# Kernel tuning notes

Hardware: AMD Instinct MI355X
Metric: run time of the kernel (lower is better)

Reference implementation:

```python
import jax, jax.numpy as jnp
import numpy as np

B, T, C, H = 256, 256, 384, 64
MAX_REL = 3  # max_relative_position hardcoded in module


def setup_inputs() -> dict:
    key = jax.random.key(0)
    ks = jax.random.split(key, 6)
    s = 1.0 / np.sqrt(C)
    return {
        "x": jax.random.normal(ks[0], (B, T, C), dtype=jnp.float32),
        "Wq": jax.random.normal(ks[1], (C, H), dtype=jnp.float32) * s,
        "Wk": jax.random.normal(ks[2], (C, H), dtype=jnp.float32) * s,
        "Wv": jax.random.normal(ks[3], (C, H), dtype=jnp.float32) * s,
        "rel_k_table": jax.random.normal(ks[4], (2 * MAX_REL + 1, H), dtype=jnp.float32) * s,
        "rel_v_table": jax.random.normal(ks[5], (2 * MAX_REL + 1, H), dtype=jnp.float32) * s,
    }


def reference(x, Wq, Wk, Wv, rel_k_table, rel_v_table):
    Bd, Td, Cd = x.shape
    Hd = Wq.shape[1]
    q = x @ Wq  # [B,T,H]
    k = x @ Wk
    v = x @ Wv
    # relative position indices, clipped Shaw-style
    r = jnp.arange(Td)
    idx = jnp.clip(r[None, :] - r[:, None], -MAX_REL, MAX_REL) + MAX_REL  # [T,T]
    rk = rel_k_table[idx]  # [T,T,H]
    rv = rel_v_table[idx]  # [T,T,H]
    attn1 = jnp.einsum('bth,bsh->bts', q, k)
    attn2 = jnp.einsum('bth,tsh->bts', q, rk)
    scale = jnp.sqrt(jnp.asarray(Hd, dtype=x.dtype))
    scores = (attn1 + attn2) / scale
    causal = jnp.tril(jnp.ones((Td, Td), dtype=bool))
    scores = jnp.where(causal[None, :, :], scores, -jnp.inf)
    attn = jax.nn.softmax(scores, axis=-1)  # dropout = identity (eval mode)
    w1 = jnp.einsum('bts,bsh->bth', attn, v)
    w2 = jnp.einsum('bts,tsh->bth', attn, rv)
    return w1 + w2  # [B,T,H]
```

## Files before the change

### kernel.cpp

```cpp
#include <hip/hip_runtime.h>
#include <hip/hip_bf16.h>


typedef __attribute__((ext_vector_type(8))) __bf16 bf16x8;
typedef __attribute__((ext_vector_type(8))) short short8;
typedef __attribute__((ext_vector_type(4))) float f32x4;
typedef __attribute__((ext_vector_type(4))) int   i32x4;

#define MFMA16(A, B, C) __builtin_amdgcn_mfma_f32_16x16x32_bf16((A), (B), (C), 0, 0, 0)

__device__ __forceinline__ unsigned short f2bf(float f) {
    unsigned int u = __builtin_bit_cast(unsigned int, f);
    u = (u + 0x7FFFu + ((u >> 16) & 1u)) >> 16;
    return (unsigned short)u;
}
__device__ __forceinline__ float bf2f(unsigned short s) {
    unsigned int u = ((unsigned int)s) << 16;
    return __builtin_bit_cast(float, u);
}
__device__ __forceinline__ bf16x8 ld16(const unsigned short* p) {
    return __builtin_bit_cast(bf16x8, *(const i32x4*)p);
}

__global__ void prep_wt(const float* __restrict__ Wq, const float* __restrict__ Wk,
                        const float* __restrict__ Wv, const float* __restrict__ relk,
                        unsigned short* __restrict__ Wt, unsigned short* __restrict__ Rk) {
    int i = blockIdx.x * 256 + threadIdx.x;
    if (i < 3 * 64 * 384) {
        int kk = i % 384;
        int h  = (i / 384) & 63;
        int w  = i / (384 * 64);
        const float* W = (w == 0) ? Wq : ((w == 1) ? Wk : Wv);
        Wt[i] = f2bf(W[kk * 64 + h]);
    } else if (i < 3 * 64 * 384 + 1024) {
        int j = i - 3 * 64 * 384;
        int n = j >> 6, h = j & 63;
        Rk[j] = (n < 4) ? f2bf(relk[n * 64 + h]) : (unsigned short)0;
    }
}

__global__ __launch_bounds__(512) void qkv_kernel(
        const float* __restrict__ x, const unsigned short* __restrict__ Wt,
        unsigned short* __restrict__ q, unsigned short* __restrict__ k,
        unsigned short* __restrict__ vT) {
    __shared__ unsigned short wlds[192][136];

    const int tid  = threadIdx.x;
    const int wave = tid >> 6;
    const int lane = tid & 63;
    const int c    = lane & 15;
    const int quad = lane >> 4;
    const int M0   = blockIdx.x * 128;
    const int myrow = M0 + wave * 16 + c;

    f32x4 zero = {0.f, 0.f, 0.f, 0.f};
    f32x4 aq[4], ak[4], av[4];
#pragma unroll
    for (int i = 0; i < 4; i++) { aq[i] = zero; ak[i] = zero; av[i] = zero; }

    for (int ck = 0; ck < 3; ck++) {
        if (ck) __syncthreads();
#pragma unroll
        for (int it = 0; it < 6; it++) {
            int i = it * 512 + tid;
            int r = i >> 4, kc = i & 15;
            i32x4 d = *(const i32x4*)(Wt + r * 384 + ck * 128 + kc * 8);
            *(i32x4*)(&wlds[r][kc * 8]) = d;
        }
        __syncthreads();

#pragma unroll
        for (int ks = 0; ks < 4; ks++) {
            const float* xp = x + (size_t)myrow * 384 + ck * 128 + ks * 32 + quad * 8;
            f32x4 x0 = *(const f32x4*)xp;
            f32x4 x1 = *(const f32x4*)(xp + 4);
            short8 xs;
#pragma unroll
            for (int j = 0; j < 4; j++) {
                xs[j]     = (short)f2bf(x0[j]);
                xs[4 + j] = (short)f2bf(x1[j]);
            }
            bf16x8 a = __builtin_bit_cast(bf16x8, xs);

#pragma unroll
            for (int nt = 0; nt < 8; nt++) {
                bf16x8 b = ld16(&wlds[nt * 16 + c][ks * 32 + quad * 8]);
                if (nt < 4) aq[nt]     = MFMA16(a, b, aq[nt]);
                else        ak[nt - 4] = MFMA16(a, b, ak[nt - 4]);
            }
#pragma unroll
            for (int mt = 0; mt < 4; mt++) {
                bf16x8 aw = ld16(&wlds[128 + mt * 16 + c][ks * 32 + quad * 8]);
                av[mt] = MFMA16(aw, a, av[mt]);
            }
        }
    }

    const int b   = M0 >> 8;
    const int t0b = M0 & 255;
#pragma unroll
    for (int nt = 0; nt < 4; nt++) {
#pragma unroll
        for (int r = 0; r < 4; r++) {
            int row = M0 + wave * 16 + quad * 4 + r;
            q[row * 64 + nt * 16 + c] = f2bf(aq[nt][r]);
            k[row * 64 + nt * 16 + c] = f2bf(ak[nt][r]);
        }
    }
#pragma unroll
    for (int mt = 0; mt < 4; mt++) {
#pragma unroll
        for (int r = 0; r < 4; r++) {
            int h = mt * 16 + quad * 4 + r;
            vT[(b * 64 + h) * 256 + t0b + wave * 16 + c] = f2bf(av[mt][r]);
        }
    }
}

__global__ __launch_bounds__(64, 4) void attn_kernel(
        const unsigned short* __restrict__ q, const unsigned short* __restrict__ k,
        const unsigned short* __restrict__ vT, const unsigned short* __restrict__ Rk,
        const float* __restrict__ relv, float* __restrict__ out) {
    __shared__ unsigned short P[16][264];
    __shared__ float E[16][4];

    const int lane = threadIdx.x;
    const int c    = lane & 15;
    const int quad = lane >> 4;
    const int tt   = blockIdx.x;
    const int b    = blockIdx.y;
    const int t0   = tt * 16;
    const int nst  = tt + 1;

    f32x4 zero = {0.f, 0.f, 0.f, 0.f};

    float rv[4][4];
#pragma unroll
    for (int j = 0; j < 4; j++)
#pragma unroll
        for (int nt = 0; nt < 4; nt++) rv[j][nt] = relv[j * 64 + nt * 16 + c];

    const unsigned short* qp = q + (size_t)(b * 256 + t0 + c) * 64 + quad * 8;
    bf16x8 aq0 = ld16(qp);
    bf16x8 aq1 = ld16(qp + 32);

    {
        f32x4 e = zero;
        e = MFMA16(aq0, ld16(Rk + c * 64 + quad * 8), e);
        e = MFMA16(aq1, ld16(Rk + c * 64 + 32 + quad * 8), e);
        if (c < 4) {
#pragma unroll
            for (int r = 0; r < 4; r++) E[quad * 4 + r][c] = e[r];
        }
    }
    __syncthreads();
    f32x4 ef[4];
#pragma unroll
    for (int r = 0; r < 4; r++) ef[r] = *(const f32x4*)(&E[quad * 4 + r][0]);

    float l[4] = {0.f, 0.f, 0.f, 0.f};
#pragma unroll
    for (int st = 0; st < 16; st++) {
        if (st < nst) {
            const unsigned short* kp = k + (size_t)(b * 256 + st * 16 + c) * 64 + quad * 8;
            f32x4 s = zero;
            s = MFMA16(aq0, ld16(kp), s);
            s = MFMA16(aq1, ld16(kp + 32), s);
#pragma unroll
            for (int r = 0; r < 4; r++) {
                int tg = t0 + quad * 4 + r;
                int sg = st * 16 + c;
                int d  = sg - tg;
                float e = (d <= -3) ? ef[r][0] : (d == -2) ? ef[r][1]
                        : (d == -1) ? ef[r][2] : ef[r][3];
                float p = (d > 0) ? 0.f : __expf(0.125f * (s[r] + e));
                l[r] += p;
                P[quad * 4 + r][sg] = f2bf(p);
            }
        }
    }
    if (nst & 1) {
#pragma unroll
        for (int r = 0; r < 4; r++) P[quad * 4 + r][nst * 16 + c] = 0;
    }
#pragma unroll
    for (int r = 0; r < 4; r++)
#pragma unroll
        for (int ofs = 1; ofs < 16; ofs <<= 1)
            l[r] += __shfl_xor(l[r], ofs, 64);
    float rl[4];
#pragma unroll
    for (int r = 0; r < 4; r++) rl[r] = 1.0f / l[r];
    __syncthreads();

    f32x4 o[4];
#pragma unroll
    for (int nt = 0; nt < 4; nt++) o[nt] = zero;
    const int ksteps = (nst + 1) >> 1;
#pragma unroll
    for (int ks = 0; ks < 8; ks++) {
        if (ks < ksteps) {
            bf16x8 ap = ld16(&P[c][ks * 32 + quad * 8]);
#pragma unroll
            for (int nt = 0; nt < 4; nt++) {
                const unsigned short* vp = vT + (size_t)(b * 64 + nt * 16 + c) * 256
                                              + ks * 32 + quad * 8;
                o[nt] = MFMA16(ap, ld16(vp), o[nt]);
            }
        }
    }

#pragma unroll
    for (int r = 0; r < 4; r++) {
        int tl = quad * 4 + r;
        int tg = t0 + tl;
        float pa = (tg >= 2) ? bf2f(P[tl][tg - 2]) * rl[r] : 0.f;
        float pb = (tg >= 1) ? bf2f(P[tl][tg - 1]) * rl[r] : 0.f;
        float pc = bf2f(P[tl][tg]) * rl[r];
#pragma unroll
        for (int nt = 0; nt < 4; nt++) {
            float r0 = rv[0][nt];
            float w2 = r0 + pa * (rv[1][nt] - r0) + pb * (rv[2][nt] - r0)
                          + pc * (rv[3][nt] - r0);
            out[(size_t)(b * 256 + tg) * 64 + nt * 16 + c] = o[nt][r] * rl[r] + w2;
        }
    }
}

extern "C" void kernel_launch(void* const* d_in, const int* in_sizes, int n_in,
                              void* d_out, int out_size, void* d_ws, size_t ws_size,
                              hipStream_t stream) {
    const float* x    = (const float*)d_in[0];
    const float* Wq   = (const float*)d_in[1];
    const float* Wk   = (const float*)d_in[2];
    const float* Wv   = (const float*)d_in[3];
    const float* relk = (const float*)d_in[4];
    const float* relv = (const float*)d_in[5];
    float* out = (float*)d_out;

    char* ws = (char*)d_ws;
    unsigned short* q  = (unsigned short*)(ws);
    unsigned short* kk = (unsigned short*)(ws + 8388608);
    unsigned short* vT = (unsigned short*)(ws + 16777216);
    unsigned short* Wt = (unsigned short*)(ws + 25165824);
    unsigned short* Rk = (unsigned short*)(ws + 25313280);

    prep_wt<<<292, 256, 0, stream>>>(Wq, Wk, Wv, relk, Wt, Rk);
    qkv_kernel<<<512, 512, 0, stream>>>(x, Wt, q, kk, vT);
    attn_kernel<<<dim3(16, 256), 64, 0, stream>>>(q, kk, vT, Rk, relv, out);
}
```

Measured before the change: 208.5 us.

## Stage x via LDS DMA in QKV and share K/V per batch in attention

The QKV kernel now uses 64-row tiles with 256 threads and loads x into LDS via global_load_lds DMA with a swizzle. Weights are staged in 96-wide K chunks. The attention kernel now runs one block per batch, staging the full K and V^T for that batch in LDS once. Four waves then loop over query tiles, so K/V are no longer reloaded from global memory by each of the 16 tiles. This trades grid size (256 blocks) and about 100KB of LDS per block for data reuse, at the risk of load imbalance from the causal triangle and lower occupancy.

New measurement: 245.3 us. 17.6% more time.

```diff
diff --git a/kernel.cpp b/kernel.cpp
--- a/kernel.cpp
+++ b/kernel.cpp
@@ -20,6 +20,12 @@
 }
 __device__ __forceinline__ bf16x8 ld16(const unsigned short* p) {
     return __builtin_bit_cast(bf16x8, *(const i32x4*)p);
+}
+
+typedef __attribute__((address_space(1))) const unsigned int GU32;
+typedef __attribute__((address_space(3))) unsigned int LU32;
+__device__ __forceinline__ void dma16(const void* g, void* l) {
+    __builtin_amdgcn_global_load_lds((GU32*)g, (LU32*)l, 16, 0, 0);
 }
 
 __global__ void prep_wt(const float* __restrict__ Wq, const float* __restrict__ Wk,
@@ -39,190 +45,209 @@
     }
 }
 
-__global__ __launch_bounds__(512) void qkv_kernel(
+__global__ __launch_bounds__(256, 2) void qkv_kernel(
         const float* __restrict__ x, const unsigned short* __restrict__ Wt,
         unsigned short* __restrict__ q, unsigned short* __restrict__ k,
         unsigned short* __restrict__ vT) {
-    __shared__ unsigned short wlds[192][136];
+    __shared__ float xs[64 * 96];
+    __shared__ unsigned short ws[192 * 100];
 
     const int tid  = threadIdx.x;
     const int wave = tid >> 6;
     const int lane = tid & 63;
     const int c    = lane & 15;
     const int quad = lane >> 4;
-    const int M0   = blockIdx.x * 128;
-    const int myrow = M0 + wave * 16 + c;
+    const int row0 = blockIdx.x * 64;
 
     f32x4 zero = {0.f, 0.f, 0.f, 0.f};
     f32x4 aq[4], ak[4], av[4];
 #pragma unroll
     for (int i = 0; i < 4; i++) { aq[i] = zero; ak[i] = zero; av[i] = zero; }
 
-    for (int ck = 0; ck < 3; ck++) {
+    const int rloc = wave * 16 + c;
+
+    for (int ck = 0; ck < 4; ck++) {
         if (ck) __syncthreads();
 #pragma unroll
-        for (int it = 0; it < 6; it++) {
-            int i = it * 512 + tid;
-            int r = i >> 4, kc = i & 15;
-            i32x4 d = *(const i32x4*)(Wt + r * 384 + ck * 128 + kc * 8);
-            *(i32x4*)(&wlds[r][kc * 8]) = d;
+        for (int s = 0; s < 6; s++) {
+            int flat = (wave * 6 + s) * 64 + lane;
+            int r  = flat / 24;
+            int qq = flat % 24;
+            int p  = (qq & ~7) | ((qq & 7) ^ (r & 7));
+            const float* g = x + (size_t)(row0 + r) * 384 + ck * 96 + p * 4;
+            dma16(g, xs + (size_t)(wave * 6 + s) * 256);
+        }
+#pragma unroll
+        for (int it = 0; it < 9; it++) {
+            int P = it * 256 + tid;
+            int r = P / 12, pc = P % 12;
+            i32x4 d = *(const i32x4*)(Wt + r * 384 + ck * 96 + pc * 8);
+            *(i32x4*)(ws + r * 100 + pc * 8) = d;
         }
         __syncthreads();
 
 #pragma unroll
-        for (int ks = 0; ks < 4; ks++) {
-            const float* xp = x + (size_t)myrow * 384 + ck * 128 + ks * 32 + quad * 8;
-            f32x4 x0 = *(const f32x4*)xp;
-            f32x4 x1 = *(const f32x4*)(xp + 4);
-            short8 xs;
+        for (int ks = 0; ks < 3; ks++) {
+            int p0 = ks * 8 + quad * 2;
+            int q0 = (p0 & ~7) | ((p0 & 7) ^ (rloc & 7));
+            int p1 = p0 + 1;
+            int q1 = (p1 & ~7) | ((p1 & 7) ^ (rloc & 7));
+            f32x4 x0 = *(const f32x4*)(xs + rloc * 96 + q0 * 4);
+            f32x4 x1 = *(const f32x4*)(xs + rloc * 96 + q1 * 4);
+            short8 xs8;
 #pragma unroll
             for (int j = 0; j < 4; j++) {
-                xs[j]     = (short)f2bf(x0[j]);
-                xs[4 + j] = (short)f2bf(x1[j]);
-            }
-            bf16x8 a = __builtin_bit_cast(bf16x8, xs);
-
-#pragma unroll
-            for (int nt = 0; nt < 8; nt++) {
-                bf16x8 b = ld16(&wlds[nt * 16 + c][ks * 32 + quad * 8]);
-                if (nt < 4) aq[nt]     = MFMA16(a, b, aq[nt]);
-                else        ak[nt - 4] = MFMA16(a, b, ak[nt - 4]);
-            }
-#pragma unroll
-            for (int mt = 0; mt < 4; mt++) {
-                bf16x8 aw = ld16(&wlds[128 + mt * 16 + c][ks * 32 + quad * 8]);
-                av[mt] = MFMA16(aw, a, av[mt]);
-            }
-        }
-    }
-
-    const int b   = M0 >> 8;
-    const int t0b = M0 & 255;
+                xs8[j]     = (short)f2bf(x0[j]);
+                xs8[4 + j] = (short)f2bf(x1[j]);
+            }
+            bf16x8 a = __builtin_bit_cast(bf16x8, xs8);
+
+#pragma unroll
+            for (int nt = 0; nt < 4; nt++) {
+                bf16x8 bq = ld16(ws + (nt * 16 + c) * 100 + (ks * 4 + quad) * 8);
+                bf16x8 bk = ld16(ws + (64 + nt * 16 + c) * 100 + (ks * 4 + quad) * 8);
+                bf16x8 aw = ld16(ws + (128 + nt * 16 + c) * 100 + (ks * 4 + quad) * 8);
+                aq[nt] = MFMA16(a, bq, aq[nt]);
+                ak[nt] = MFMA16(a, bk, ak[nt]);
+                av[nt] = MFMA16(aw, a, av[nt]);
+            }
+        }
+    }
+
+    const int b   = row0 >> 8;
+    const int t0b = row0 & 255;
 #pragma unroll
     for (int nt = 0; nt < 4; nt++) {
 #pragma unroll
         for (int r = 0; r < 4; r++) {
-            int row = M0 + wave * 16 + quad * 4 + r;
+            int row = row0 + wave * 16 + quad * 4 + r;
             q[row * 64 + nt * 16 + c] = f2bf(aq[nt][r]);
             k[row * 64 + nt * 16 + c] = f2bf(ak[nt][r]);
-        }
-    }
-#pragma unroll
-    for (int mt = 0; mt < 4; mt++) {
-#pragma unroll
-        for (int r = 0; r < 4; r++) {
-            int h = mt * 16 + quad * 4 + r;
-            vT[(b * 64 + h) * 256 + t0b + wave * 16 + c] = f2bf(av[mt][r]);
-        }
-    }
-}
-
-__global__ __launch_bounds__(64, 4) void attn_kernel(
-        const unsigned short* __restrict__ q, const unsigned short* __restrict__ k,
+            int h = nt * 16 + quad * 4 + r;
+            vT[(b * 64 + h) * 256 + t0b + wave * 16 + c] = f2bf(av[nt][r]);
+        }
+    }
+}
+
+__global__ __launch_bounds__(256) void attn_kernel(
+        const unsigned short* __restrict__ q, const unsigned short* __restrict__ kg,
         const unsigned short* __restrict__ vT, const unsigned short* __restrict__ Rk,
         const float* __restrict__ relv, float* __restrict__ out) {
-    __shared__ unsigned short P[16][264];
-    __shared__ float E[16][4];
-
-    const int lane = threadIdx.x;
+    extern __shared__ char smem[];
+    unsigned short* kb = (unsigned short*)(smem);
+    unsigned short* vb = (unsigned short*)(smem + 34816);
+    unsigned short* Pb = (unsigned short*)(smem + 68608);
+
+    const int tid  = threadIdx.x;
+    const int wave = tid >> 6;
+    const int lane = tid & 63;
     const int c    = lane & 15;
     const int quad = lane >> 4;
-    const int tt   = blockIdx.x;
-    const int b    = blockIdx.y;
-    const int t0   = tt * 16;
-    const int nst  = tt + 1;
+    const int b    = blockIdx.x;
 
     f32x4 zero = {0.f, 0.f, 0.f, 0.f};
 
+#pragma unroll
+    for (int it = 0; it < 8; it++) {
+        int P = it * 256 + tid;
+        int r = P >> 3, pc = P & 7;
+        i32x4 d = *(const i32x4*)(kg + ((size_t)b * 256 + r) * 64 + pc * 8);
+        *(i32x4*)(kb + r * 68 + pc * 8) = d;
+    }
+#pragma unroll
+    for (int it = 0; it < 8; it++) {
+        int P = it * 256 + tid;
+        int r = P >> 5, pc = P & 31;
+        i32x4 d = *(const i32x4*)(vT + ((size_t)b * 64 + r) * 256 + pc * 8);
+        *(i32x4*)(vb + r * 264 + pc * 8) = d;
+    }
+    __syncthreads();
+
+    bf16x8 rk0 = ld16(Rk + c * 64 + quad * 8);
+    bf16x8 rk1 = ld16(Rk + c * 64 + 32 + quad * 8);
     float rv[4][4];
 #pragma unroll
     for (int j = 0; j < 4; j++)
 #pragma unroll
         for (int nt = 0; nt < 4; nt++) rv[j][nt] = relv[j * 64 + nt * 16 + c];
-
-    const unsigned short* qp = q + (size_t)(b * 256 + t0 + c) * 64 + quad * 8;
-    bf16x8 aq0 = ld16(qp);
-    bf16x8 aq1 = ld16(qp + 32);
-
-    {
-        f32x4 e = zero;
-        e = MFMA16(aq0, ld16(Rk + c * 64 + quad * 8), e);
-        e = MFMA16(aq1, ld16(Rk + c * 64 + 32 + quad * 8), e);
-        if (c < 4) {
-#pragma unroll
-            for (int r = 0; r < 4; r++) E[quad * 4 + r][c] = e[r];
-        }
-    }
-    __syncthreads();
-    f32x4 ef[4];
-#pragma unroll
-    for (int r = 0; r < 4; r++) ef[r] = *(const f32x4*)(&E[quad * 4 + r][0]);
-
-    float l[4] = {0.f, 0.f, 0.f, 0.f};
-#pragma unroll
-    for (int st = 0; st < 16; st++) {
-        if (st < nst) {
-            const unsigned short* kp = k + (size_t)(b * 256 + st * 16 + c) * 64 + quad * 8;
-            f32x4 s = zero;
-            s = MFMA16(aq0, ld16(kp), s);
-            s = MFMA16(aq1, ld16(kp + 32), s);
+    unsigned short* Pw = Pb + wave * 16 * 264;
+
+    for (int ti = 0; ti < 4; ti++) {
+        const int tt  = ti * 4 + wave;
+        const int t0  = tt * 16;
+        const int nst = tt + 1;
+
+        const unsigned short* qp = q + (size_t)(b * 256 + t0 + c) * 64 + quad * 8;
+        bf16x8 aq0 = ld16(qp);
+        bf16x8 aq1 = ld16(qp + 32);
+
+        f32x4 e = MFMA16(aq0, rk0, zero);
+        e = MFMA16(aq1, rk1, e);
+        float ef[4][4];
+#pragma unroll
+        for (int r = 0; r < 4; r++)
+#pragma unroll
+            for (int j = 0; j < 4; j++)
+                ef[r][j] = __shfl(e[r], (lane & 48) | j, 64);
+
+        float l[4] = {0.f, 0.f, 0.f, 0.f};
+        for (int st = 0; st < nst; st++) {
+            int R = st * 16 + c;
+            f32x4 s = MFMA16(aq0, ld16(kb + R * 68 + quad * 8), zero);
+            s = MFMA16(aq1, ld16(kb + R * 68 + 32 + quad * 8), s);
 #pragma unroll
             for (int r = 0; r < 4; r++) {
                 int tg = t0 + quad * 4 + r;
-                int sg = st * 16 + c;
-                int d  = sg - tg;
-                float e = (d <= -3) ? ef[r][0] : (d == -2) ? ef[r][1]
-                        : (d == -1) ? ef[r][2] : ef[r][3];
-                float p = (d > 0) ? 0.f : __expf(0.125f * (s[r] + e));
+                int d  = R - tg;
+                float ee = (d <= -3) ? ef[r][0] : (d == -2) ? ef[r][1]
+                         : (d == -1) ? ef[r][2] : ef[r][3];
+                float p = (d > 0) ? 0.f : __expf(0.125f * (s[r] + ee));
                 l[r] += p;
-                P[quad * 4 + r][sg] = f2bf(p);
-            }
-        }
-    }
-    if (nst & 1) {
-#pragma unroll
-        for (int r = 0; r < 4; r++) P[quad * 4 + r][nst * 16 + c] = 0;
-    }
-#pragma unroll
-    for (int r = 0; r < 4; r++)
-#pragma unroll
-        for (int ofs = 1; ofs < 16; ofs <<= 1)
-            l[r] += __shfl_xor(l[r], ofs, 64);
-    float rl[4];
-#pragma unroll
-    for (int r = 0; r < 4; r++) rl[r] = 1.0f / l[r];
-    __syncthreads();
-
-    f32x4 o[4];
-#pragma unroll
-    for (int nt = 0; nt < 4; nt++) o[nt] = zero;
-    const int ksteps = (nst + 1) >> 1;
-#pragma unroll
-    for (int ks = 0; ks < 8; ks++) {
-        if (ks < ksteps) {
-            bf16x8 ap = ld16(&P[c][ks * 32 + quad * 8]);
+                Pw[(quad * 4 + r) * 264 + R] = f2bf(p);
+            }
+        }
+        if (nst & 1) {
+#pragma unroll
+            for (int r = 0; r < 4; r++) Pw[(quad * 4 + r) * 264 + nst * 16 + c] = 0;
+        }
+#pragma unroll
+        for (int r = 0; r < 4; r++)
+#pragma unroll
+            for (int ofs = 1; ofs < 16; ofs <<= 1)
+                l[r] += __shfl_xor(l[r], ofs, 64);
+        float rl[4];
+#pragma unroll
+        for (int r = 0; r < 4; r++) rl[r] = 1.0f / l[r];
+
+        __asm__ volatile("s_waitcnt lgkmcnt(0)" ::: "memory");
+
+        f32x4 o[4];
+#pragma unroll
+        for (int nt = 0; nt < 4; nt++) o[nt] = zero;
+        const int ksteps = (nst + 1) >> 1;
+        for (int ks = 0; ks < ksteps; ks++) {
+            bf16x8 ap = ld16(Pw + c * 264 + ks * 32 + quad * 8);
 #pragma unroll
             for (int nt = 0; nt < 4; nt++) {
-                const unsigned short* vp = vT + (size_t)(b * 64 + nt * 16 + c) * 256
-                                              + ks * 32 + quad * 8;
-                o[nt] = MFMA16(ap, ld16(vp), o[nt]);
-            }
-        }
-    }
-
-#pragma unroll
-    for (int r = 0; r < 4; r++) {
-        int tl = quad * 4 + r;
-        int tg = t0 + tl;
-        float pa = (tg >= 2) ? bf2f(P[tl][tg - 2]) * rl[r] : 0.f;
-        float pb = (tg >= 1) ? bf2f(P[tl][tg - 1]) * rl[r] : 0.f;
-        float pc = bf2f(P[tl][tg]) * rl[r];
-#pragma unroll
-        for (int nt = 0; nt < 4; nt++) {
-            float r0 = rv[0][nt];
-            float w2 = r0 + pa * (rv[1][nt] - r0) + pb * (rv[2][nt] - r0)
-                          + pc * (rv[3][nt] - r0);
-            out[(size_t)(b * 256 + tg) * 64 + nt * 16 + c] = o[nt][r] * rl[r] + w2;
+                bf16x8 vf = ld16(vb + (nt * 16 + c) * 264 + ks * 32 + quad * 8);
+                o[nt] = MFMA16(ap, vf, o[nt]);
+            }
+        }
+
+#pragma unroll
+        for (int r = 0; r < 4; r++) {
+            int tl = quad * 4 + r;
+            int tg = t0 + tl;
+            float pa = (tg >= 2) ? bf2f(Pw[tl * 264 + tg - 2]) * rl[r] : 0.f;
+            float pb = (tg >= 1) ? bf2f(Pw[tl * 264 + tg - 1]) * rl[r] : 0.f;
+            float pc = bf2f(Pw[tl * 264 + tg]) * rl[r];
+#pragma unroll
+            for (int nt = 0; nt < 4; nt++) {
+                float r0 = rv[0][nt];
+                float w2 = r0 + pa * (rv[1][nt] - r0) + pb * (rv[2][nt] - r0)
+                              + pc * (rv[3][nt] - r0);
+                out[(size_t)(b * 256 + tg) * 64 + nt * 16 + c] = o[nt][r] * rl[r] + w2;
+            }
         }
     }
 }
@@ -245,7 +270,10 @@
     unsigned short* Wt = (unsigned short*)(ws + 25165824);
     unsigned short* Rk = (unsigned short*)(ws + 25313280);
 
+    (void)hipFuncSetAttribute((const void*)attn_kernel,
+                              hipFuncAttributeMaxDynamicSharedMemorySize, 102400);
+
     prep_wt<<<292, 256, 0, stream>>>(Wq, Wk, Wv, relk, Wt, Rk);
-    qkv_kernel<<<512, 512, 0, stream>>>(x, Wt, q, kk, vT);
-    attn_kernel<<<dim3(16, 256), 64, 0, stream>>>(q, kk, vT, Rk, relv, out);
-}
+    qkv_kernel<<<1024, 256, 0, stream>>>(x, Wt, q, kk, vT);
+    attn_kernel<<<256, 256, 102400, stream>>>(q, kk, vT, Rk, relv, out);
+}
```
